# Kernel optimization log

Hardware: AMD Instinct MI355X
Metric: run time of the kernel (lower is better)

The kernel has to match this reference:

```python
import jax, jax.numpy as jnp
import numpy as np

VOCAB, S, D, H, DH, L, W1S, DFF = 50265, 4096, 768, 12, 64, 2, 256, 3072


def layer_norm(x, g, b, eps=1e-5):
    m = jnp.mean(x, axis=-1, keepdims=True)
    v = jnp.mean((x - m) ** 2, axis=-1, keepdims=True)
    return (x - m) * jax.lax.rsqrt(v + eps) * g + b


def sliding_global_attn(q, k, v, att, w=W1S):
    # q,k,v: [B,H,S,Dh]; att: [B,S] float (1 real / 0 pad). Longformer-style
    # sliding window (one-sided w) + global attention on token 0.
    B, nh, S_, Dh = q.shape
    nc = S_ // w
    q = q * (Dh ** -0.5)
    k_pad = jnp.pad(k, ((0, 0), (0, 0), (w, w), (0, 0)))
    v_pad = jnp.pad(v, ((0, 0), (0, 0), (w, w), (0, 0)))
    idx = jnp.arange(nc)[:, None] * w + jnp.arange(3 * w)[None, :]  # [nc,3w] into padded axis
    k_band = k_pad[:, :, idx]  # [B,H,nc,3w,Dh]
    v_band = v_pad[:, :, idx]
    qc = q.reshape(B, nh, nc, w, Dh)
    s_loc = jnp.einsum('bhcqd,bhckd->bhcqk', qc, k_band)  # [B,H,nc,w,3w]
    rel = jnp.arange(3 * w)[None, :] - jnp.arange(w)[:, None]  # [w,3w]
    band_ok = (rel >= 0) & (rel <= 2 * w)
    key_abs = idx - w  # [nc,3w] absolute key positions
    in_seq = (key_abs >= 0) & (key_abs < S_) & (key_abs != 0)  # token 0 handled by global column
    key_real = att[:, jnp.clip(key_abs, 0, S_ - 1)] > 0  # [B,nc,3w]
    valid = band_ok[None, None, None] & in_seq[None, None, :, None, :] & key_real[:, None, :, None, :]
    s_loc = jnp.where(valid, s_loc, -1e9)
    s_g = jnp.einsum('bhcqd,bhd->bhcq', qc, k[:, :, 0])  # global key column
    p = jax.nn.softmax(jnp.concatenate([s_g[..., None], s_loc], axis=-1), axis=-1)
    out = (jnp.einsum('bhcq,bhd->bhcqd', p[..., 0], v[:, :, 0])
           + jnp.einsum('bhcqk,bhckd->bhcqd', p[..., 1:], v_band)).reshape(B, nh, S_, Dh)
    # global token 0 attends to everything
    s0 = jnp.where(att[:, None, :] > 0, jnp.einsum('bhd,bhsd->bhs', q[:, :, 0], k), -1e9)
    out0 = jnp.einsum('bhs,bhsd->bhd', jax.nn.softmax(s0, axis=-1), v)
    return out.at[:, :, 0].set(out0)


def setup_inputs() -> dict:
    key = jax.random.key(0)
    ks = jax.random.split(key, 16)
    sc = 0.02
    inp = {
        'input_ids': jax.random.randint(ks[0], (2, S), 0, VOCAB, dtype=jnp.int64)
        if jax.config.jax_enable_x64 else jax.random.randint(ks[0], (2, S), 0, VOCAB, dtype=jnp.int32),
        'attention_mask': jnp.ones((2, S), dtype=jnp.int32),
        'word_emb': sc * jax.random.normal(ks[1], (VOCAB, D), jnp.float32),
        'pos_emb': sc * jax.random.normal(ks[2], (S, D), jnp.float32),
        'emb_ln_g': jnp.ones((D,), jnp.float32), 'emb_ln_b': jnp.zeros((D,), jnp.float32),
        'Wq': sc * jax.random.normal(ks[3], (L, D, D), jnp.float32), 'bq': jnp.zeros((L, D), jnp.float32),
        'Wk': sc * jax.random.normal(ks[4], (L, D, D), jnp.float32), 'bk': jnp.zeros((L, D), jnp.float32),
        'Wv': sc * jax.random.normal(ks[5], (L, D, D), jnp.float32), 'bv': jnp.zeros((L, D), jnp.float32),
        'Wo': sc * jax.random.normal(ks[6], (L, D, D), jnp.float32), 'bo': jnp.zeros((L, D), jnp.float32),
        'ln1_g': jnp.ones((L, D), jnp.float32), 'ln1_b': jnp.zeros((L, D), jnp.float32),
        'Wf1': sc * jax.random.normal(ks[7], (L, D, DFF), jnp.float32), 'bf1': jnp.zeros((L, DFF), jnp.float32),
        'Wf2': sc * jax.random.normal(ks[8], (L, DFF, D), jnp.float32), 'bf2': jnp.zeros((L, D), jnp.float32),
        'ln2_g': jnp.ones((L, D), jnp.float32), 'ln2_b': jnp.zeros((L, D), jnp.float32),
        'Wh1': sc * jax.random.normal(ks[9], (D, 256), jnp.float32), 'bh1': jnp.zeros((256,), jnp.float32),
        'Wh2': sc * jax.random.normal(ks[10], (256, 14), jnp.float32), 'bh2': jnp.zeros((14,), jnp.float32),
    }
    return inp


def reference(input_ids, attention_mask, word_emb, pos_emb, emb_ln_g, emb_ln_b,
              Wq, bq, Wk, bk, Wv, bv, Wo, bo, ln1_g, ln1_b,
              Wf1, bf1, Wf2, bf2, ln2_g, ln2_b, Wh1, bh1, Wh2, bh2):
    B, S_ = input_ids.shape
    att = attention_mask.astype(jnp.float32)
    x = word_emb[input_ids] + pos_emb[None, :S_, :]
    x = layer_norm(x, emb_ln_g, emb_ln_b)
    for l in range(L):
        def heads(w, b):
            return (x @ w + b).reshape(B, S_, H, DH).transpose(0, 2, 1, 3)
        q = heads(Wq[l], bq[l]); k = heads(Wk[l], bk[l]); v = heads(Wv[l], bv[l])
        a = sliding_global_attn(q, k, v, att)
        a = a.transpose(0, 2, 1, 3).reshape(B, S_, D) @ Wo[l] + bo[l]
        x = layer_norm(x + a, ln1_g[l], ln1_b[l])
        f = jax.nn.gelu(x @ Wf1[l] + bf1[l]) @ Wf2[l] + bf2[l]
        x = layer_norm(x + f, ln2_g[l], ln2_b[l])
    # masked mean pool
    m = att[..., None]
    pooled = jnp.sum(x * m, axis=1) / jnp.clip(jnp.sum(m, axis=1), 1e-9)
    h = jax.nn.relu(pooled @ Wh1 + bh1)
    return jax.nn.sigmoid(h @ Wh2 + bh2) * 4.0
```

## Files before the change

kernel.cpp:

```cpp
#include <hip/hip_runtime.h>
#include <hip/hip_bf16.h>
#include <math.h>

#define S_LEN 4096
#define D_MODEL 768
#define NHEAD 12
#define DH 64
#define NLAYER 2
#define DFF 3072
#define BATCH 2
#define QSTR 2304

typedef __attribute__((ext_vector_type(8))) __bf16 bf16x8;
typedef __attribute__((ext_vector_type(4))) float f32x4;

__device__ __forceinline__ unsigned short f2bf_bits(float f) {
  unsigned int u = __float_as_uint(f);
  unsigned int r = (u + 0x7fffu + ((u >> 16) & 1u)) >> 16;
  return (unsigned short)r;
}

__device__ __forceinline__ float bf2f(unsigned short u) {
  return __uint_as_float(((unsigned int)u) << 16);
}

__device__ __forceinline__ unsigned int cvtpk_bf16(float lo, float hi) {
  unsigned int d;
  asm("v_cvt_pk_bf16_f32 %0, %1, %2" : "=v"(d) : "v"(lo), "v"(hi));
  return d;
}

#define ASYNC_COPY16(gsrc, ldst)                                       \
  __builtin_amdgcn_global_load_lds(                                    \
      (const __attribute__((address_space(1))) void*)(gsrc),           \
      (__attribute__((address_space(3))) void*)(ldst), 16, 0, 0)

#define MFMA_BF16(a, b, c) __builtin_amdgcn_mfma_f32_16x16x32_bf16(a, b, c, 0, 0, 0)

__device__ __forceinline__ float blk_sum256(float v, float* lds) {
#pragma unroll
  for (int off = 32; off > 0; off >>= 1) v += __shfl_down(v, off, 64);
  __syncthreads();
  if ((threadIdx.x & 63) == 0) lds[threadIdx.x >> 6] = v;
  __syncthreads();
  return lds[0] + lds[1] + lds[2] + lds[3];
}

__global__ __launch_bounds__(256) void wconv_kernel(
    const float* __restrict__ Wq, const float* __restrict__ Wk,
    const float* __restrict__ Wv, const float* __restrict__ Wo,
    const float* __restrict__ Wf1, const float* __restrict__ Wf2,
    unsigned short* __restrict__ Wbf) {
  int id = blockIdx.x;
  const float* src;
  unsigned short* dst;
  int K, N, t;
  if (id < 4608) {
    int m = id / 576;
    t = id % 576;
    int layer = m >> 2, which = m & 3;
    const float* s = (which == 0) ? Wq : (which == 1) ? Wk : (which == 2) ? Wv : Wo;
    src = s + (size_t)layer * 589824;
    dst = Wbf + (size_t)layer * 7077888 + (size_t)which * 589824;
    K = 768; N = 768;
  } else if (id < 9216) {
    int j = id - 4608;
    int layer = j / 2304;
    t = j % 2304;
    src = Wf1 + (size_t)layer * 2359296;
    dst = Wbf + (size_t)layer * 7077888 + 2359296;
    K = 768; N = 3072;
  } else {
    int j = id - 9216;
    int layer = j / 2304;
    t = j % 2304;
    src = Wf2 + (size_t)layer * 2359296;
    dst = Wbf + (size_t)layer * 7077888 + 4718592;
    K = 3072; N = 768;
  }
  int tiles_n = N >> 5;
  int tk = t / tiles_n, tn = t % tiles_n;
  __shared__ float tile[32][33];
  int c = threadIdx.x & 31, r0 = threadIdx.x >> 5;
#pragma unroll
  for (int p = 0; p < 4; ++p) {
    int r = r0 + p * 8;
    tile[r][c] = src[(size_t)(tk * 32 + r) * N + tn * 32 + c];
  }
  __syncthreads();
#pragma unroll
  for (int p = 0; p < 4; ++p) {
    int r = r0 + p * 8;
    dst[(size_t)(tn * 32 + r) * K + tk * 32 + c] = f2bf_bits(tile[c][r]);
  }
}

__global__ __launch_bounds__(256) void embed_ln_kernel(
    const int* __restrict__ ids, const float* __restrict__ wemb,
    const float* __restrict__ pemb, const float* __restrict__ g,
    const float* __restrict__ b, float* __restrict__ X,
    unsigned short* __restrict__ Xb) {
  int row = blockIdx.x;
  int s = row % S_LEN;
  int id = ids[row];
  const float* we = wemb + (size_t)id * D_MODEL;
  const float* pe = pemb + (size_t)s * D_MODEL;
  int t = threadIdx.x;
  __shared__ float lds[4];
  float v0 = we[t] + pe[t];
  float v1 = we[t + 256] + pe[t + 256];
  float v2 = we[t + 512] + pe[t + 512];
  float mean = blk_sum256(v0 + v1 + v2, lds) * (1.f / 768.f);
  float d0 = v0 - mean, d1 = v1 - mean, d2 = v2 - mean;
  float var = blk_sum256(d0 * d0 + d1 * d1 + d2 * d2, lds) * (1.f / 768.f);
  float rs = rsqrtf(var + 1e-5f);
  float o0 = d0 * rs * g[t] + b[t];
  float o1 = d1 * rs * g[t + 256] + b[t + 256];
  float o2 = d2 * rs * g[t + 512] + b[t + 512];
  float* xp = X + (size_t)row * D_MODEL;
  xp[t] = o0; xp[t + 256] = o1; xp[t + 512] = o2;
  unsigned short* xb = Xb + (size_t)row * D_MODEL;
  xb[t] = f2bf_bits(o0); xb[t + 256] = f2bf_bits(o1); xb[t + 512] = f2bf_bits(o2);
}

__global__ __launch_bounds__(256) void ln_kernel(
    const float* __restrict__ T, const float* __restrict__ g,
    const float* __restrict__ b, float* __restrict__ X,
    unsigned short* __restrict__ Xb) {
  int row = blockIdx.x;
  const float* tp = T + (size_t)row * D_MODEL;
  int t = threadIdx.x;
  __shared__ float lds[4];
  float v0 = tp[t], v1 = tp[t + 256], v2 = tp[t + 512];
  float mean = blk_sum256(v0 + v1 + v2, lds) * (1.f / 768.f);
  float d0 = v0 - mean, d1 = v1 - mean, d2 = v2 - mean;
  float var = blk_sum256(d0 * d0 + d1 * d1 + d2 * d2, lds) * (1.f / 768.f);
  float rs = rsqrtf(var + 1e-5f);
  float o0 = d0 * rs * g[t] + b[t];
  float o1 = d1 * rs * g[t + 256] + b[t + 256];
  float o2 = d2 * rs * g[t + 512] + b[t + 512];
  float* xp = X + (size_t)row * D_MODEL;
  xp[t] = o0; xp[t + 256] = o1; xp[t + 512] = o2;
  unsigned short* xb = Xb + (size_t)row * D_MODEL;
  xb[t] = f2bf_bits(o0); xb[t + 256] = f2bf_bits(o1); xb[t + 512] = f2bf_bits(o2);
}

template <int MODE>
__global__ __launch_bounds__(256) void gemm_bf16(
    const unsigned short* __restrict__ A, const unsigned short* __restrict__ Bt,
    const float* __restrict__ bias0, const float* __restrict__ bias1,
    const float* __restrict__ bias2, const float* __restrict__ Res,
    void* __restrict__ Cout, int M, int N, int K) {
  __shared__ unsigned short Abuf[3][128 * 32];
  __shared__ unsigned short Bbuf[3][128 * 32];
  const int tid = threadIdx.x;
  const int lane = tid & 63, w = tid >> 6;
  const int wm = w >> 1, wn = w & 1;

  const int nbx = gridDim.x;
  const int nwg = nbx * gridDim.y;
  const int orig = blockIdx.y * nbx + blockIdx.x;
  const int wgid = (orig & 7) * (nwg >> 3) + (orig >> 3);
  const int m0 = (wgid / nbx) * 128, n0 = (wgid % nbx) * 128;

  f32x4 acc[4][4];
#pragma unroll
  for (int i = 0; i < 4; ++i)
#pragma unroll
    for (int j = 0; j < 4; ++j) acc[i][j] = (f32x4){0.f, 0.f, 0.f, 0.f};

  const int s0 = w * 64 + lane, s1 = s0 + 256;
  const int r0 = s0 >> 2, c0 = (s0 & 3) ^ (r0 & 3);
  const int r1 = s1 >> 2, c1 = (s1 & 3) ^ (r1 & 3);
  const unsigned short* gA0 = A + (size_t)(m0 + r0) * K + c0 * 8;
  const unsigned short* gA1 = A + (size_t)(m0 + r1) * K + c1 * 8;
  const unsigned short* gB0 = Bt + (size_t)(n0 + r0) * K + c0 * 8;
  const unsigned short* gB1 = Bt + (size_t)(n0 + r1) * K + c1 * 8;
  const int dA0 = (w * 64) * 8, dA1 = (256 + w * 64) * 8;

  const int frow = lane & 15, kgrp = lane >> 4;
  int aoff[4], boff[4];
#pragma unroll
  for (int i = 0; i < 4; ++i) {
    int ra = wm * 64 + i * 16 + frow;
    int rb = wn * 64 + i * 16 + frow;
    aoff[i] = ra * 32 + ((kgrp ^ (ra & 3)) * 8);
    boff[i] = rb * 32 + ((kgrp ^ (rb & 3)) * 8);
  }

#define STAGE(bsel)                                                       \
  {                                                                       \
    ASYNC_COPY16(gA0, &Abuf[bsel][dA0]);                                  \
    ASYNC_COPY16(gA1, &Abuf[bsel][dA1]);                                  \
    ASYNC_COPY16(gB0, &Bbuf[bsel][dA0]);                                  \
    ASYNC_COPY16(gB1, &Bbuf[bsel][dA1]);                                  \
    gA0 += 32; gA1 += 32; gB0 += 32; gB1 += 32;                           \
  }

  const int nk = K >> 5;
  STAGE(0);
  if (nk > 1) STAGE(1);
  asm volatile("s_waitcnt vmcnt(4)" ::: "memory");
  __builtin_amdgcn_s_barrier();
  __builtin_amdgcn_sched_barrier(0);

  int cur = 0;
  for (int kt = 0; kt < nk; ++kt) {
    if (kt + 2 < nk) {
      int nxt = cur + 2;
      if (nxt >= 3) nxt -= 3;
      STAGE(nxt);
    }
    bf16x8 av[4], bv[4];
#pragma unroll
    for (int i = 0; i < 4; ++i) av[i] = *(const bf16x8*)(&Abuf[cur][aoff[i]]);
#pragma unroll
    for (int j = 0; j < 4; ++j) bv[j] = *(const bf16x8*)(&Bbuf[cur][boff[j]]);
#pragma unroll
    for (int i = 0; i < 4; ++i)
#pragma unroll
      for (int j = 0; j < 4; ++j)
        acc[i][j] = MFMA_BF16(av[i], bv[j], acc[i][j]);
    if (kt + 1 < nk) {
      if (kt + 2 < nk)
        asm volatile("s_waitcnt vmcnt(4)" ::: "memory");
      else
        asm volatile("s_waitcnt vmcnt(0)" ::: "memory");
      __builtin_amdgcn_s_barrier();
      __builtin_amdgcn_sched_barrier(0);
    }
    cur = (cur == 2) ? 0 : cur + 1;
  }
#undef STAGE

#pragma unroll
  for (int i = 0; i < 4; ++i) {
#pragma unroll
    for (int j = 0; j < 4; ++j) {
      int grb = m0 + wm * 64 + i * 16 + (lane >> 4) * 4;
      int gc = n0 + wn * 64 + j * 16 + (lane & 15);
      float bsv;
      if (MODE == 4)
        bsv = (gc < 768) ? bias0[gc] : (gc < 1536) ? bias1[gc - 768] : bias2[gc - 1536];
      else
        bsv = bias0[gc];
#pragma unroll
      for (int r = 0; r < 4; ++r) {
        int gr = grb + r;
        float v = acc[i][j][r] + bsv;
        if (MODE == 1) {
          float x = v;
          float th = tanhf(0.7978845608028654f * (x + 0.044715f * x * x * x));
          v = 0.5f * x * (1.f + th);
        }
        if (MODE == 4 && gc < 768) v *= 0.125f;
        if (MODE == 2) v += Res[(size_t)gr * N + gc];
        if (MODE == 1 || MODE == 4)
          ((unsigned short*)Cout)[(size_t)gr * N + gc] = f2bf_bits(v);
        else
          ((float*)Cout)[(size_t)gr * N + gc] = v;
      }
    }
  }
}

__global__ __launch_bounds__(256) void vtrans_kernel(
    const unsigned short* __restrict__ Vsrc, unsigned short* __restrict__ Vt) {
  int kb = blockIdx.x, h = blockIdx.y, b = blockIdx.z;
  int k0 = kb * 64;
  const size_t bs = (size_t)b * S_LEN;
  const size_t bh = (size_t)(b * NHEAD + h);
  __shared__ unsigned short tile[64][72];
  int tid = threadIdx.x;
#pragma unroll
  for (int p = 0; p < 2; ++p) {
    int idx = p * 256 + tid;
    int key = idx >> 3, ch = idx & 7;
    bf16x8 v = *(const bf16x8*)(Vsrc + (bs + k0 + key) * QSTR + h * DH + ch * 8);
    *(bf16x8*)&tile[key][ch * 8] = v;
  }
  __syncthreads();
#pragma unroll
  for (int p = 0; p < 2; ++p) {
    int idx = p * 256 + tid;
    int d = idx >> 3, kc = idx & 7;
    unsigned int w0 = tile[kc * 8 + 0][d] | ((unsigned int)tile[kc * 8 + 1][d] << 16);
    unsigned int w1 = tile[kc * 8 + 2][d] | ((unsigned int)tile[kc * 8 + 3][d] << 16);
    unsigned int w2 = tile[kc * 8 + 4][d] | ((unsigned int)tile[kc * 8 + 5][d] << 16);
    unsigned int w3 = tile[kc * 8 + 6][d] | ((unsigned int)tile[kc * 8 + 7][d] << 16);
    uint4 out = make_uint4(w0, w1, w2, w3);
    *(uint4*)(Vt + (bh * 64 + d) * S_LEN + k0 + kc * 8) = out;
  }
}

__global__ __launch_bounds__(512) void band_attn_kernel(
    const unsigned short* __restrict__ Qg, const unsigned short* __restrict__ Kgb,
    const unsigned short* __restrict__ Vgb, const unsigned short* __restrict__ Vt,
    const int* __restrict__ att, unsigned short* __restrict__ Aout) {
  const int c = blockIdx.x, h = blockIdx.y, b = blockIdx.z;
  const int tid = threadIdx.x;
  const int lane = tid & 63, wq = tid >> 6;
  const int g = lane >> 4, cl = lane & 15;
  const size_t bs = (size_t)b * S_LEN;
  const size_t bh = (size_t)(b * NHEAD + h);

  __shared__ __align__(16) char smem[18944];

  if (c == 16) {
    float* sc = (float*)smem;
    float* q0 = sc + S_LEN;
    float* red = q0 + 64;
    float* part = red + 8;
    if (tid < 64) q0[tid] = bf2f(Qg[bs * QSTR + h * DH + tid]);
    __syncthreads();
    float lmax = -1e30f;
    for (int s = tid; s < S_LEN; s += 512) {
      const unsigned short* kp = Kgb + (bs + s) * QSTR + h * DH;
      float acc = 0.f;
#pragma unroll
      for (int cc = 0; cc < 8; ++cc) {
        uint4 u = *(const uint4*)(kp + cc * 8);
        const unsigned int* uu = (const unsigned int*)&u;
#pragma unroll
        for (int w2 = 0; w2 < 4; ++w2) {
          unsigned int x = uu[w2];
          acc += q0[cc * 8 + w2 * 2] * __uint_as_float(x << 16);
          acc += q0[cc * 8 + w2 * 2 + 1] * __uint_as_float(x & 0xffff0000u);
        }
      }
      acc = (att[b * S_LEN + s] > 0) ? acc : -1e9f;
      sc[s] = acc;
      lmax = fmaxf(lmax, acc);
    }
#pragma unroll
    for (int off = 32; off > 0; off >>= 1) lmax = fmaxf(lmax, __shfl_down(lmax, off, 64));
    __syncthreads();
    if (lane == 0) red[wq] = lmax;
    __syncthreads();
    float M = red[0];
#pragma unroll
    for (int i = 1; i < 8; ++i) M = fmaxf(M, red[i]);
    float lsum = 0.f;
    for (int s = tid; s < S_LEN; s += 512) {
      float p = __expf(sc[s] - M);
      sc[s] = p;
      lsum += p;
    }
#pragma unroll
    for (int off = 32; off > 0; off >>= 1) lsum += __shfl_down(lsum, off, 64);
    __syncthreads();
    if (lane == 0) red[wq] = lsum;
    __syncthreads();
    float L = red[0];
#pragma unroll
    for (int i = 1; i < 8; ++i) L += red[i];
    int d = tid & 63, chunk = tid >> 6;
    float acc2 = 0.f;
    for (int s = chunk * 512; s < (chunk + 1) * 512; ++s)
      acc2 += sc[s] * bf2f(Vgb[(bs + s) * QSTR + h * DH + d]);
    part[chunk * 64 + d] = acc2;
    __syncthreads();
    if (tid < 64) {
      float v = 0.f;
#pragma unroll
      for (int i = 0; i < 8; ++i) v += part[i * 64 + tid];
      Aout[bs * D_MODEL + h * DH + tid] = f2bf_bits(v / L);
    }
    return;
  }

  unsigned short* Klds = (unsigned short*)smem;
  unsigned short* Vlds = Klds + 64 * 64;
  float* kmask = (float*)(Vlds + 64 * 64);

  bf16x8 qf[2][2];
#pragma unroll
  for (int qt = 0; qt < 2; ++qt)
#pragma unroll
    for (int ks = 0; ks < 2; ++ks)
      qf[qt][ks] = *(const bf16x8*)(Qg + (bs + c * 256 + wq * 32 + qt * 16 + cl) * QSTR +
                                    h * DH + ks * 32 + g * 8);

  float mrun[2], lrun[2];
  f32x4 oacc[2][4];
#pragma unroll
  for (int qt = 0; qt < 2; ++qt) {
    float sg = 0.f;
#pragma unroll
    for (int ks = 0; ks < 2; ++ks) {
      bf16x8 k0 = *(const bf16x8*)(Kgb + bs * QSTR + h * DH + ks * 32 + g * 8);
#pragma unroll
      for (int j = 0; j < 8; ++j) sg += (float)qf[qt][ks][j] * (float)k0[j];
    }
    sg += __shfl_xor(sg, 16, 64);
    sg += __shfl_xor(sg, 32, 64);
    mrun[qt] = sg;
    lrun[qt] = 1.f;
  }
#pragma unroll
  for (int dt = 0; dt < 4; ++dt) {
    float v0d = bf2f(Vgb[bs * QSTR + h * DH + dt * 16 + cl]);
    f32x4 vv = {v0d, v0d, v0d, v0d};
    oacc[0][dt] = vv;
    oacc[1][dt] = vv;
  }

  const int jlo = wq * 32, jhi = wq * 32 + 543;

  for (int t = 0; t < 12; ++t) {
    int kabs0 = c * 256 - 256 + t * 64;
    if (kabs0 < 0 || kabs0 >= S_LEN) continue;
    __syncthreads();
    {
      int key = tid >> 3, ch = tid & 7;
      bf16x8 kv = *(const bf16x8*)(Kgb + (bs + kabs0 + key) * QSTR + h * DH + ch * 8);
      *(bf16x8*)(Klds + key * 64 + ((ch ^ (key & 7)) * 8)) = kv;
      bf16x8 vv = *(const bf16x8*)(Vt + (bh * 64 + key) * S_LEN + kabs0 + ch * 8);
      *(bf16x8*)(Vlds + key * 64 + ((ch ^ (key & 7)) * 8)) = vv;
      if (tid < 64) {
        int ka = kabs0 + tid;
        kmask[tid] = (ka >= 1 && att[b * S_LEN + ka] > 0) ? 0.f : -1e9f;
      }
    }
    __syncthreads();
    if (t * 64 + 63 < jlo || t * 64 > jhi) continue;

    f32x4 accs[4][2];
#pragma unroll
    for (int kt = 0; kt < 4; ++kt) {
      accs[kt][0] = (f32x4){0.f, 0.f, 0.f, 0.f};
      accs[kt][1] = (f32x4){0.f, 0.f, 0.f, 0.f};
    }
#pragma unroll
    for (int ks = 0; ks < 2; ++ks) {
      bf16x8 kf[4];
#pragma unroll
      for (int kt = 0; kt < 4; ++kt) {
        int key = kt * 16 + cl;
        kf[kt] = *(const bf16x8*)(Klds + key * 64 + (((ks * 4 + g) ^ (key & 7)) * 8));
      }
#pragma unroll
      for (int kt = 0; kt < 4; ++kt) {
        accs[kt][0] = MFMA_BF16(kf[kt], qf[0][ks], accs[kt][0]);
        accs[kt][1] = MFMA_BF16(kf[kt], qf[1][ks], accs[kt][1]);
      }
    }

#pragma unroll
    for (int qt = 0; qt < 2; ++qt) {
      int iq = wq * 32 + qt * 16 + cl;
      int relbase = t * 64 - iq;
      float pvv[4][4];
      float tmax = -1e30f;
#pragma unroll
      for (int kt = 0; kt < 4; ++kt)
#pragma unroll
        for (int r = 0; r < 4; ++r) {
          int key = kt * 16 + g * 4 + r;
          int rel = relbase + key;
          float x = accs[kt][qt][r] + kmask[key];
          x = (rel >= 0 && rel <= 512) ? x : -1e9f;
          pvv[kt][r] = x;
          tmax = fmaxf(tmax, x);
        }
      tmax = fmaxf(tmax, __shfl_xor(tmax, 16, 64));
      tmax = fmaxf(tmax, __shfl_xor(tmax, 32, 64));
      float mnew = fmaxf(mrun[qt], tmax);
      float scale = __expf(mrun[qt] - mnew);
      mrun[qt] = mnew;
      float psum = 0.f;
#pragma unroll
      for (int kt = 0; kt < 4; ++kt)
#pragma unroll
        for (int r = 0; r < 4; ++r) {
          float p = __expf(pvv[kt][r] - mnew);
          pvv[kt][r] = p;
          psum += p;
        }
      psum += __shfl_xor(psum, 16, 64);
      psum += __shfl_xor(psum, 32, 64);
      lrun[qt] = lrun[qt] * scale + psum;
      float scr[4];
#pragma unroll
      for (int r = 0; r < 4; ++r) scr[r] = __shfl(scale, g * 4 + r, 64);
#pragma unroll
      for (int dt = 0; dt < 4; ++dt) {
        oacc[qt][dt][0] *= scr[0];
        oacc[qt][dt][1] *= scr[1];
        oacc[qt][dt][2] *= scr[2];
        oacc[qt][dt][3] *= scr[3];
      }
#pragma unroll
      for (int ks = 0; ks < 2; ++ks) {
        unsigned int E0D0 = cvtpk_bf16(pvv[ks * 2][0], pvv[ks * 2][1]);
        unsigned int E0D1 = cvtpk_bf16(pvv[ks * 2][2], pvv[ks * 2][3]);
        unsigned int E1D0 = cvtpk_bf16(pvv[ks * 2 + 1][0], pvv[ks * 2 + 1][1]);
        unsigned int E1D1 = cvtpk_bf16(pvv[ks * 2 + 1][2], pvv[ks * 2 + 1][3]);
        int src0 = ((lane >> 4) & 1) * 32 + cl;
        int src1 = src0 + 16;
        unsigned int a0 = (unsigned int)__shfl((int)E0D0, src0, 64);
        unsigned int a1 = (unsigned int)__shfl((int)E0D1, src0, 64);
        unsigned int a2 = (unsigned int)__shfl((int)E0D0, src1, 64);
        unsigned int a3 = (unsigned int)__shfl((int)E0D1, src1, 64);
        unsigned int b0 = (unsigned int)__shfl((int)E1D0, src0, 64);
        unsigned int b1 = (unsigned int)__shfl((int)E1D1, src0, 64);
        unsigned int b2 = (unsigned int)__shfl((int)E1D0, src1, 64);
        unsigned int b3 = (unsigned int)__shfl((int)E1D1, src1, 64);
        bool hi = lane >= 32;
        union { unsigned int u[4]; bf16x8 v; } af;
        af.u[0] = hi ? b0 : a0;
        af.u[1] = hi ? b1 : a1;
        af.u[2] = hi ? b2 : a2;
        af.u[3] = hi ? b3 : a3;
#pragma unroll
        for (int dt = 0; dt < 4; ++dt) {
          int d = dt * 16 + cl;
          bf16x8 vf = *(const bf16x8*)(Vlds + d * 64 + (((ks * 4 + g) ^ (d & 7)) * 8));
          oacc[qt][dt] = MFMA_BF16(af.v, vf, oacc[qt][dt]);
        }
      }
    }
  }

#pragma unroll
  for (int qt = 0; qt < 2; ++qt) {
    float lr[4];
#pragma unroll
    for (int r = 0; r < 4; ++r) lr[r] = 1.f / __shfl(lrun[qt], g * 4 + r, 64);
#pragma unroll
    for (int dt = 0; dt < 4; ++dt)
#pragma unroll
      for (int r = 0; r < 4; ++r) {
        int row = c * 256 + wq * 32 + qt * 16 + g * 4 + r;
        if (row != 0)
          Aout[(bs + row) * D_MODEL + h * DH + dt * 16 + cl] =
              f2bf_bits(oacc[qt][dt][r] * lr[r]);
      }
  }
}

__global__ __launch_bounds__(256) void pool1_kernel(
    const float* __restrict__ X, const int* __restrict__ att,
    float* __restrict__ ppart) {
  int sb = blockIdx.x, b = blockIdx.y, t = threadIdx.x;
  float a0 = 0.f, a1 = 0.f, a2 = 0.f;
  for (int s = sb * 256; s < sb * 256 + 256; ++s) {
    float a = (float)att[b * S_LEN + s];
    const float* xp = X + ((size_t)b * S_LEN + s) * D_MODEL;
    a0 += xp[t] * a; a1 += xp[t + 256] * a; a2 += xp[t + 512] * a;
  }
  float* pp = ppart + ((size_t)b * 16 + sb) * D_MODEL;
  pp[t] = a0; pp[t + 256] = a1; pp[t + 512] = a2;
}

__global__ __launch_bounds__(256) void pool2_kernel(
    const float* __restrict__ ppart, const int* __restrict__ att,
    float* __restrict__ pooled) {
  int b = blockIdx.x, t = threadIdx.x;
  float a0 = 0.f, a1 = 0.f, a2 = 0.f;
  for (int sb = 0; sb < 16; ++sb) {
    const float* pp = ppart + ((size_t)b * 16 + sb) * D_MODEL;
    a0 += pp[t]; a1 += pp[t + 256]; a2 += pp[t + 512];
  }
  float cnt = 0.f;
  for (int s = 0; s < S_LEN; ++s) cnt += (float)att[b * S_LEN + s];
  cnt = fmaxf(cnt, 1e-9f);
  pooled[b * D_MODEL + t]       = a0 / cnt;
  pooled[b * D_MODEL + t + 256] = a1 / cnt;
  pooled[b * D_MODEL + t + 512] = a2 / cnt;
}

__global__ __launch_bounds__(256) void head_kernel(
    const float* __restrict__ pooled, const float* __restrict__ Wh1,
    const float* __restrict__ bh1, const float* __restrict__ Wh2,
    const float* __restrict__ bh2, float* __restrict__ out) {
  __shared__ float hbuf[2][256];
  int t = threadIdx.x;
  for (int b = 0; b < 2; ++b) {
    float acc = bh1[t];
    for (int d = 0; d < D_MODEL; ++d) acc += pooled[b * D_MODEL + d] * Wh1[d * 256 + t];
    hbuf[b][t] = fmaxf(acc, 0.f);
  }
  __syncthreads();
  if (t < 28) {
    int b = t / 14, j = t % 14;
    float acc = bh2[j];
    for (int i = 0; i < 256; ++i) acc += hbuf[b][i] * Wh2[i * 14 + j];
    out[t] = 4.f / (1.f + __expf(-acc));
  }
}

extern "C" void kernel_launch(void* const* d_in, const int* in_sizes, int n_in,
                              void* d_out, int out_size, void* d_ws,
                              size_t ws_size, hipStream_t stream) {
  const int* ids    = (const int*)d_in[0];
  const int* att    = (const int*)d_in[1];
  const float* wemb = (const float*)d_in[2];
  const float* pemb = (const float*)d_in[3];
  const float* elng = (const float*)d_in[4];
  const float* elnb = (const float*)d_in[5];
  const float* Wq   = (const float*)d_in[6];
  const float* bq   = (const float*)d_in[7];
  const float* Wk   = (const float*)d_in[8];
  const float* bk   = (const float*)d_in[9];
  const float* Wv   = (const float*)d_in[10];
  const float* bv   = (const float*)d_in[11];
  const float* Wo   = (const float*)d_in[12];
  const float* bo   = (const float*)d_in[13];
  const float* ln1g = (const float*)d_in[14];
  const float* ln1b = (const float*)d_in[15];
  const float* Wf1  = (const float*)d_in[16];
  const float* bf1  = (const float*)d_in[17];
  const float* Wf2  = (const float*)d_in[18];
  const float* bf2  = (const float*)d_in[19];
  const float* ln2g = (const float*)d_in[20];
  const float* ln2b = (const float*)d_in[21];
  const float* Wh1  = (const float*)d_in[22];
  const float* bh1  = (const float*)d_in[23];
  const float* Wh2  = (const float*)d_in[24];
  const float* bh2  = (const float*)d_in[25];

  const int M = BATCH * S_LEN;
  float* ws = (float*)d_ws;
  float* X  = ws;
  float* T  = ws + 6291456;
  unsigned short* QKV = (unsigned short*)(ws + 12582912);
  unsigned short* Vt  = (unsigned short*)(ws + 22020096);
  unsigned short* FFbf = QKV;
  unsigned short* Abbf = (unsigned short*)(ws + 23592960);
  unsigned short* Xbf  = (unsigned short*)(ws + 26738688);
  unsigned short* Wbf  = (unsigned short*)(ws + 29884416);
  float* pooled = ws + 36962304;
  float* ppart  = ws + 36963840;

  wconv_kernel<<<13824, 256, 0, stream>>>(Wq, Wk, Wv, Wo, Wf1, Wf2, Wbf);
  embed_ln_kernel<<<M, 256, 0, stream>>>(ids, wemb, pemb, elng, elnb, X, Xbf);

  for (int l = 0; l < NLAYER; ++l) {
    const unsigned short* wqkv = Wbf + (size_t)l * 7077888;
    const unsigned short* wot  = wqkv + 1769472;
    const unsigned short* wf1t = wqkv + 2359296;
    const unsigned short* wf2t = wqkv + 4718592;

    gemm_bf16<4><<<dim3(18, 64), 256, 0, stream>>>(
        Xbf, wqkv, bq + l * D_MODEL, bk + l * D_MODEL, bv + l * D_MODEL,
        nullptr, QKV, M, QSTR, 768);

    vtrans_kernel<<<dim3(64, NHEAD, BATCH), 256, 0, stream>>>(QKV + 1536, Vt);
    band_attn_kernel<<<dim3(17, NHEAD, BATCH), 512, 0, stream>>>(
        QKV, QKV + 768, QKV + 1536, Vt, att, Abbf);

    gemm_bf16<2><<<dim3(6, 64), 256, 0, stream>>>(
        Abbf, wot, bo + l * D_MODEL, nullptr, nullptr, X, T, M, 768, 768);
    ln_kernel<<<M, 256, 0, stream>>>(T, ln1g + l * D_MODEL, ln1b + l * D_MODEL, X, Xbf);

    gemm_bf16<1><<<dim3(24, 64), 256, 0, stream>>>(
        Xbf, wf1t, bf1 + l * DFF, nullptr, nullptr, nullptr, FFbf, M, DFF, 768);
    gemm_bf16<2><<<dim3(6, 64), 256, 0, stream>>>(
        FFbf, wf2t, bf2 + l * D_MODEL, nullptr, nullptr, X, T, M, 768, DFF);
    ln_kernel<<<M, 256, 0, stream>>>(T, ln2g + l * D_MODEL, ln2b + l * D_MODEL, X, Xbf);
  }

  pool1_kernel<<<dim3(16, BATCH), 256, 0, stream>>>(X, att, ppart);
  pool2_kernel<<<BATCH, 256, 0, stream>>>(ppart, att, pooled);
  head_kernel<<<1, 256, 0, stream>>>(pooled, Wh1, bh1, Wh2, bh2, (float*)d_out);
}
```

Measured before the change: 876.1 us.

## Use 32x32 MFMA GEMMs, bf16 residual stream, and fast exp-based GELU

```diff
diff --git a/kernel.cpp b/kernel.cpp
--- a/kernel.cpp
+++ b/kernel.cpp
@@ -13,6 +13,7 @@
 
 typedef __attribute__((ext_vector_type(8))) __bf16 bf16x8;
 typedef __attribute__((ext_vector_type(4))) float f32x4;
+typedef __attribute__((ext_vector_type(16))) float f32x16;
 
 __device__ __forceinline__ unsigned short f2bf_bits(float f) {
   unsigned int u = __float_as_uint(f);
@@ -30,12 +31,20 @@
   return d;
 }
 
+__device__ __forceinline__ float gelu_fast(float x) {
+  float u = 0.7978845608028654f * (x + 0.044715f * x * x * x);
+  float t2 = fminf(fmaxf(2.f * u, -18.f), 18.f);
+  float e = __expf(t2);
+  return 0.5f * x * (1.f + (e - 1.f) / (e + 1.f));
+}
+
 #define ASYNC_COPY16(gsrc, ldst)                                       \
   __builtin_amdgcn_global_load_lds(                                    \
       (const __attribute__((address_space(1))) void*)(gsrc),           \
       (__attribute__((address_space(3))) void*)(ldst), 16, 0, 0)
 
 #define MFMA_BF16(a, b, c) __builtin_amdgcn_mfma_f32_16x16x32_bf16(a, b, c, 0, 0, 0)
+#define MFMA32_BF16(a, b, c) __builtin_amdgcn_mfma_f32_32x32x16_bf16(a, b, c, 0, 0, 0)
 
 __device__ __forceinline__ float blk_sum256(float v, float* lds) {
 #pragma unroll
@@ -98,8 +107,7 @@
 __global__ __launch_bounds__(256) void embed_ln_kernel(
     const int* __restrict__ ids, const float* __restrict__ wemb,
     const float* __restrict__ pemb, const float* __restrict__ g,
-    const float* __restrict__ b, float* __restrict__ X,
-    unsigned short* __restrict__ Xb) {
+    const float* __restrict__ b, unsigned short* __restrict__ Xb) {
   int row = blockIdx.x;
   int s = row % S_LEN;
   int id = ids[row];
@@ -114,19 +122,15 @@
   float d0 = v0 - mean, d1 = v1 - mean, d2 = v2 - mean;
   float var = blk_sum256(d0 * d0 + d1 * d1 + d2 * d2, lds) * (1.f / 768.f);
   float rs = rsqrtf(var + 1e-5f);
-  float o0 = d0 * rs * g[t] + b[t];
-  float o1 = d1 * rs * g[t + 256] + b[t + 256];
-  float o2 = d2 * rs * g[t + 512] + b[t + 512];
-  float* xp = X + (size_t)row * D_MODEL;
-  xp[t] = o0; xp[t + 256] = o1; xp[t + 512] = o2;
   unsigned short* xb = Xb + (size_t)row * D_MODEL;
-  xb[t] = f2bf_bits(o0); xb[t + 256] = f2bf_bits(o1); xb[t + 512] = f2bf_bits(o2);
+  xb[t]       = f2bf_bits(d0 * rs * g[t] + b[t]);
+  xb[t + 256] = f2bf_bits(d1 * rs * g[t + 256] + b[t + 256]);
+  xb[t + 512] = f2bf_bits(d2 * rs * g[t + 512] + b[t + 512]);
 }
 
 __global__ __launch_bounds__(256) void ln_kernel(
     const float* __restrict__ T, const float* __restrict__ g,
-    const float* __restrict__ b, float* __restrict__ X,
-    unsigned short* __restrict__ Xb) {
+    const float* __restrict__ b, unsigned short* __restrict__ Xb) {
   int row = blockIdx.x;
   const float* tp = T + (size_t)row * D_MODEL;
   int t = threadIdx.x;
@@ -136,21 +140,142 @@
   float d0 = v0 - mean, d1 = v1 - mean, d2 = v2 - mean;
   float var = blk_sum256(d0 * d0 + d1 * d1 + d2 * d2, lds) * (1.f / 768.f);
   float rs = rsqrtf(var + 1e-5f);
-  float o0 = d0 * rs * g[t] + b[t];
-  float o1 = d1 * rs * g[t + 256] + b[t + 256];
-  float o2 = d2 * rs * g[t + 512] + b[t + 512];
-  float* xp = X + (size_t)row * D_MODEL;
-  xp[t] = o0; xp[t + 256] = o1; xp[t + 512] = o2;
   unsigned short* xb = Xb + (size_t)row * D_MODEL;
-  xb[t] = f2bf_bits(o0); xb[t + 256] = f2bf_bits(o1); xb[t + 512] = f2bf_bits(o2);
+  xb[t]       = f2bf_bits(d0 * rs * g[t] + b[t]);
+  xb[t + 256] = f2bf_bits(d1 * rs * g[t + 256] + b[t + 256]);
+  xb[t + 512] = f2bf_bits(d2 * rs * g[t + 512] + b[t + 512]);
 }
 
 template <int MODE>
-__global__ __launch_bounds__(256) void gemm_bf16(
+__global__ __launch_bounds__(256) void gemm32(
     const unsigned short* __restrict__ A, const unsigned short* __restrict__ Bt,
     const float* __restrict__ bias0, const float* __restrict__ bias1,
-    const float* __restrict__ bias2, const float* __restrict__ Res,
+    const float* __restrict__ bias2, const unsigned short* __restrict__ ResBf,
     void* __restrict__ Cout, int M, int N, int K) {
+  __shared__ unsigned short Abuf[3][128 * 32];
+  __shared__ unsigned short Bbuf[3][128 * 32];
+  const int tid = threadIdx.x;
+  const int lane = tid & 63, w = tid >> 6;
+  const int wm = w >> 1, wn = w & 1;
+  const int l31 = lane & 31, l5 = lane >> 5;
+
+  const int nbx = gridDim.x;
+  const int nwg = nbx * gridDim.y;
+  const int orig = blockIdx.y * nbx + blockIdx.x;
+  const int wgid = (orig & 7) * (nwg >> 3) + (orig >> 3);
+  const int m0 = (wgid / nbx) * 128, n0 = (wgid % nbx) * 128;
+
+  f32x16 acc[2][2];
+#pragma unroll
+  for (int i = 0; i < 2; ++i)
+#pragma unroll
+    for (int j = 0; j < 2; ++j)
+#pragma unroll
+      for (int r = 0; r < 16; ++r) acc[i][j][r] = 0.f;
+
+  const int s0 = w * 64 + lane, s1 = s0 + 256;
+  const int r0 = s0 >> 2, c0 = (s0 & 3) ^ ((r0 >> 1) & 3);
+  const int r1 = s1 >> 2, c1 = (s1 & 3) ^ ((r1 >> 1) & 3);
+  const unsigned short* gA0 = A + (size_t)(m0 + r0) * K + c0 * 8;
+  const unsigned short* gA1 = A + (size_t)(m0 + r1) * K + c1 * 8;
+  const unsigned short* gB0 = Bt + (size_t)(n0 + r0) * K + c0 * 8;
+  const unsigned short* gB1 = Bt + (size_t)(n0 + r1) * K + c1 * 8;
+  const int dA0 = (w * 64) * 8, dA1 = (256 + w * 64) * 8;
+
+  int aoff[2][2], boff[2][2];
+#pragma unroll
+  for (int mt = 0; mt < 2; ++mt) {
+    int ra = wm * 64 + mt * 32 + l31;
+    int rb = wn * 64 + mt * 32 + l31;
+    int key_a = (ra >> 1) & 3, key_b = (rb >> 1) & 3;
+#pragma unroll
+    for (int ks = 0; ks < 2; ++ks) {
+      aoff[mt][ks] = ra * 32 + ((((ks << 1) | l5) ^ key_a) << 3);
+      boff[mt][ks] = rb * 32 + ((((ks << 1) | l5) ^ key_b) << 3);
+    }
+  }
+
+#define STAGE(bsel)                                                       \
+  {                                                                       \
+    ASYNC_COPY16(gA0, &Abuf[bsel][dA0]);                                  \
+    ASYNC_COPY16(gA1, &Abuf[bsel][dA1]);                                  \
+    ASYNC_COPY16(gB0, &Bbuf[bsel][dA0]);                                  \
+    ASYNC_COPY16(gB1, &Bbuf[bsel][dA1]);                                  \
+    gA0 += 32; gA1 += 32; gB0 += 32; gB1 += 32;                           \
+  }
+
+  const int nk = K >> 5;
+  STAGE(0);
+  if (nk > 1) STAGE(1);
+  asm volatile("s_waitcnt vmcnt(4)" ::: "memory");
+  __builtin_amdgcn_s_barrier();
+  __builtin_amdgcn_sched_barrier(0);
+
+  int cur = 0;
+  for (int kt = 0; kt < nk; ++kt) {
+    if (kt + 2 < nk) {
+      int nxt = cur + 2;
+      if (nxt >= 3) nxt -= 3;
+      STAGE(nxt);
+    }
+    bf16x8 av[2][2], bv[2][2];
+#pragma unroll
+    for (int mt = 0; mt < 2; ++mt)
+#pragma unroll
+      for (int ks = 0; ks < 2; ++ks) {
+        av[mt][ks] = *(const bf16x8*)(&Abuf[cur][aoff[mt][ks]]);
+        bv[mt][ks] = *(const bf16x8*)(&Bbuf[cur][boff[mt][ks]]);
+      }
+#pragma unroll
+    for (int mt = 0; mt < 2; ++mt)
+#pragma unroll
+      for (int nt = 0; nt < 2; ++nt)
+#pragma unroll
+        for (int ks = 0; ks < 2; ++ks)
+          acc[mt][nt] = MFMA32_BF16(av[mt][ks], bv[nt][ks], acc[mt][nt]);
+    if (kt + 1 < nk) {
+      if (kt + 2 < nk)
+        asm volatile("s_waitcnt vmcnt(4)" ::: "memory");
+      else
+        asm volatile("s_waitcnt vmcnt(0)" ::: "memory");
+      __builtin_amdgcn_s_barrier();
+      __builtin_amdgcn_sched_barrier(0);
+    }
+    cur = (cur == 2) ? 0 : cur + 1;
+  }
+#undef STAGE
+
+#pragma unroll
+  for (int mt = 0; mt < 2; ++mt) {
+#pragma unroll
+    for (int nt = 0; nt < 2; ++nt) {
+      int gc = n0 + wn * 64 + nt * 32 + l31;
+      float bsv;
+      if (MODE == 4)
+        bsv = (gc < 768) ? bias0[gc] : (gc < 1536) ? bias1[gc - 768] : bias2[gc - 1536];
+      else
+        bsv = bias0[gc];
+#pragma unroll
+      for (int reg = 0; reg < 16; ++reg) {
+        int gr = m0 + wm * 64 + mt * 32 + (reg & 3) + 8 * (reg >> 2) + 4 * l5;
+        float v = acc[mt][nt][reg] + bsv;
+        if (MODE == 1) v = gelu_fast(v);
+        if (MODE == 4 && gc < 768) v *= 0.125f;
+        if (MODE == 2) {
+          v += bf2f(ResBf[(size_t)gr * 768 + gc]);
+          ((float*)Cout)[(size_t)gr * N + gc] = v;
+        } else {
+          ((unsigned short*)Cout)[(size_t)gr * N + gc] = f2bf_bits(v);
+        }
+      }
+    }
+  }
+}
+
+__global__ __launch_bounds__(256) void gemm_bf16_m1(
+    const unsigned short* __restrict__ A, const unsigned short* __restrict__ Bt,
+    const float* __restrict__ bias0, unsigned short* __restrict__ Cout,
+    int M, int N, int K) {
   __shared__ unsigned short Abuf[3][128 * 32];
   __shared__ unsigned short Bbuf[3][128 * 32];
   const int tid = threadIdx.x;
@@ -239,26 +364,11 @@
     for (int j = 0; j < 4; ++j) {
       int grb = m0 + wm * 64 + i * 16 + (lane >> 4) * 4;
       int gc = n0 + wn * 64 + j * 16 + (lane & 15);
-      float bsv;
-      if (MODE == 4)
-        bsv = (gc < 768) ? bias0[gc] : (gc < 1536) ? bias1[gc - 768] : bias2[gc - 1536];
-      else
-        bsv = bias0[gc];
+      float bsv = bias0[gc];
 #pragma unroll
       for (int r = 0; r < 4; ++r) {
-        int gr = grb + r;
-        float v = acc[i][j][r] + bsv;
-        if (MODE == 1) {
-          float x = v;
-          float th = tanhf(0.7978845608028654f * (x + 0.044715f * x * x * x));
-          v = 0.5f * x * (1.f + th);
-        }
-        if (MODE == 4 && gc < 768) v *= 0.125f;
-        if (MODE == 2) v += Res[(size_t)gr * N + gc];
-        if (MODE == 1 || MODE == 4)
-          ((unsigned short*)Cout)[(size_t)gr * N + gc] = f2bf_bits(v);
-        else
-          ((float*)Cout)[(size_t)gr * N + gc] = v;
+        float v = gelu_fast(acc[i][j][r] + bsv);
+        Cout[(size_t)(grb + r) * N + gc] = f2bf_bits(v);
       }
     }
   }
@@ -540,14 +650,14 @@
 }
 
 __global__ __launch_bounds__(256) void pool1_kernel(
-    const float* __restrict__ X, const int* __restrict__ att,
+    const unsigned short* __restrict__ Xb, const int* __restrict__ att,
     float* __restrict__ ppart) {
   int sb = blockIdx.x, b = blockIdx.y, t = threadIdx.x;
   float a0 = 0.f, a1 = 0.f, a2 = 0.f;
   for (int s = sb * 256; s < sb * 256 + 256; ++s) {
     float a = (float)att[b * S_LEN + s];
-    const float* xp = X + ((size_t)b * S_LEN + s) * D_MODEL;
-    a0 += xp[t] * a; a1 += xp[t + 256] * a; a2 += xp[t + 512] * a;
+    const unsigned short* xp = Xb + ((size_t)b * S_LEN + s) * D_MODEL;
+    a0 += bf2f(xp[t]) * a; a1 += bf2f(xp[t + 256]) * a; a2 += bf2f(xp[t + 512]) * a;
   }
   float* pp = ppart + ((size_t)b * 16 + sb) * D_MODEL;
   pp[t] = a0; pp[t + 256] = a1; pp[t + 512] = a2;
@@ -622,19 +732,18 @@
 
   const int M = BATCH * S_LEN;
   float* ws = (float*)d_ws;
-  float* X  = ws;
-  float* T  = ws + 6291456;
-  unsigned short* QKV = (unsigned short*)(ws + 12582912);
-  unsigned short* Vt  = (unsigned short*)(ws + 22020096);
-  unsigned short* FFbf = QKV;
-  unsigned short* Abbf = (unsigned short*)(ws + 23592960);
-  unsigned short* Xbf  = (unsigned short*)(ws + 26738688);
-  unsigned short* Wbf  = (unsigned short*)(ws + 29884416);
-  float* pooled = ws + 36962304;
-  float* ppart  = ws + 36963840;
+  float* T = ws;
+  unsigned short* QKV  = (unsigned short*)(ws + 6291456);
+  unsigned short* Vt   = (unsigned short*)(ws + 11010048);
+  unsigned short* Abbf = (unsigned short*)(ws + 12582912);
+  unsigned short* Xbf  = (unsigned short*)(ws + 15728640);
+  unsigned short* FFbf = (unsigned short*)(ws + 18874368);
+  unsigned short* Wbf  = (unsigned short*)(ws + 31457280);
+  float* pooled = ws + 38535168;
+  float* ppart  = ws + 38536704;
 
   wconv_kernel<<<13824, 256, 0, stream>>>(Wq, Wk, Wv, Wo, Wf1, Wf2, Wbf);
-  embed_ln_kernel<<<M, 256, 0, stream>>>(ids, wemb, pemb, elng, elnb, X, Xbf);
+  embed_ln_kernel<<<M, 256, 0, stream>>>(ids, wemb, pemb, elng, elnb, Xbf);
 
   for (int l = 0; l < NLAYER; ++l) {
     const unsigned short* wqkv = Wbf + (size_t)l * 7077888;
@@ -642,7 +751,7 @@
     const unsigned short* wf1t = wqkv + 2359296;
     const unsigned short* wf2t = wqkv + 4718592;
 
-    gemm_bf16<4><<<dim3(18, 64), 256, 0, stream>>>(
+    gemm32<4><<<dim3(18, 64), 256, 0, stream>>>(
         Xbf, wqkv, bq + l * D_MODEL, bk + l * D_MODEL, bv + l * D_MODEL,
         nullptr, QKV, M, QSTR, 768);
 
@@ -650,18 +759,23 @@
     band_attn_kernel<<<dim3(17, NHEAD, BATCH), 512, 0, stream>>>(
         QKV, QKV + 768, QKV + 1536, Vt, att, Abbf);
 
-    gemm_bf16<2><<<dim3(6, 64), 256, 0, stream>>>(
-        Abbf, wot, bo + l * D_MODEL, nullptr, nullptr, X, T, M, 768, 768);
-    ln_kernel<<<M, 256, 0, stream>>>(T, ln1g + l * D_MODEL, ln1b + l * D_MODEL, X, Xbf);
-
-    gemm_bf16<1><<<dim3(24, 64), 256, 0, stream>>>(
-        Xbf, wf1t, bf1 + l * DFF, nullptr, nullptr, nullptr, FFbf, M, DFF, 768);
-    gemm_bf16<2><<<dim3(6, 64), 256, 0, stream>>>(
-        FFbf, wf2t, bf2 + l * D_MODEL, nullptr, nullptr, X, T, M, 768, DFF);
-    ln_kernel<<<M, 256, 0, stream>>>(T, ln2g + l * D_MODEL, ln2b + l * D_MODEL, X, Xbf);
-  }
-
-  pool1_kernel<<<dim3(16, BATCH), 256, 0, stream>>>(X, att, ppart);
+    gemm32<2><<<dim3(6, 64), 256, 0, stream>>>(
+        Abbf, wot, bo + l * D_MODEL, nullptr, nullptr, Xbf, T, M, 768, 768);
+    ln_kernel<<<M, 256, 0, stream>>>(T, ln1g + l * D_MODEL, ln1b + l * D_MODEL, Xbf);
+
+    if (l == 0)
+      gemm_bf16_m1<<<dim3(24, 64), 256, 0, stream>>>(
+          Xbf, wf1t, bf1 + l * DFF, FFbf, M, DFF, 768);
+    else
+      gemm32<1><<<dim3(24, 64), 256, 0, stream>>>(
+          Xbf, wf1t, bf1 + l * DFF, nullptr, nullptr, nullptr, FFbf, M, DFF, 768);
+
+    gemm32<2><<<dim3(6, 64), 256, 0, stream>>>(
+        FFbf, wf2t, bf2 + l * D_MODEL, nullptr, nullptr, Xbf, T, M, 768, DFF);
+    ln_kernel<<<M, 256, 0, stream>>>(T, ln2g + l * D_MODEL, ln2b + l * D_MODEL, Xbf);
+  }
+
+  pool1_kernel<<<dim3(16, BATCH), 256, 0, stream>>>(Xbf, att, ppart);
   pool2_kernel<<<BATCH, 256, 0, stream>>>(ppart, att, pooled);
   head_kernel<<<1, 256, 0, stream>>>(pooled, Wh1, bh1, Wh2, bh2, (float*)d_out);
 }
```

Result: faster. 830.8 us (-5.2%).
